# Performance work log

Hardware: AMD Instinct MI355X
Metric: run time of the kernel (lower is better)

The kernel has to match this reference:

```python
import jax, jax.numpy as jnp
import numpy as np

B, D, P, E, C = 2048, 4096, 64, 8, 64
K = D // P  # conv kernel = stride = input_dim / patch_num


def setup_inputs() -> dict:
    key = jax.random.key(0)
    k1, k2, k3, k4 = jax.random.split(key, 4)
    x = jax.random.normal(k1, (B, 1, D), jnp.float32)
    router_w = jax.random.normal(k2, (E, K), jnp.float32) * 0.02   # Router conv weight [E,1,K] squeezed
    expert_w = jax.random.normal(k3, (E, 2 * C, K), jnp.float32) * 0.001  # per-expert conv weights (small=True scaling)
    expert_b = jax.random.normal(k4, (E, 2 * C), jnp.float32) * 0.001
    return {"x": x, "router_w": router_w, "expert_w": expert_w, "expert_b": expert_b}


def reference(x, router_w, expert_w, expert_b):
    b, _, d = x.shape
    e, k = router_w.shape
    p = d // k
    c = expert_w.shape[1] // 2

    # Conv1d(1, ch, K, stride=K) == per-patch matmul; sum over dim 2 == sum over patches.
    patches = x.reshape(b, p, k)                                   # [B,P,K]

    # Router (eval mode: no noise)
    select = jnp.einsum('bpk,ek->be', patches, router_w)           # [B,E]

    # top1 routing
    gate = jnp.max(select, axis=-1)                                # [B]
    index = jnp.argmax(select, axis=-1)                            # [B]
    onehot = jax.nn.one_hot(index, e, dtype=select.dtype)          # [B,E]

    # aux load-balance loss
    density = onehot.mean(axis=0)
    density_proxy = select.mean(axis=0)
    loss = (density_proxy * density).mean() * float(e ** 2)

    # combine/dispatch (mask_flat is all ones for top1)
    combine = gate[:, None] * onehot                               # [B,E]
    dispatch = jax.lax.stop_gradient((combine != 0).astype(select.dtype))  # bool cast detaches grad
    select0 = dispatch

    # Dense dispatch: every expert sees the full batch, zero-masked by dispatch.
    # z[e,b,c,p] = conv of (dispatch[b,e]*x[b]) with expert e's kernel, + bias
    z = jnp.einsum('bpk,eck->ebcp', patches, expert_w)             # [E,B,2C,P]
    z = z * dispatch.T[:, :, None, None] + expert_b[:, None, :, None]
    z = z ** 3                                                     # nonlinear=True
    s = z.sum(axis=-1)                                             # sum over patches -> [E,B,2C]
    expert_out = jnp.stack([s[..., :c].sum(-1), s[..., c:].sum(-1)], axis=-1)  # [E,B,2]

    out = jnp.einsum('be,ebl->bl', combine, expert_out)            # [B,2]
    out = jax.nn.softmax(out, axis=1)
    return out, select0, loss
```

## Files before the change

### kernel.cpp

```cpp
#include <hip/hip_runtime.h>

#define BB 2048
#define DD 4096
#define PP 64
#define KK 64
#define EE 8
#define C2 128
#define NBLK (BB / 2)

typedef __attribute__((ext_vector_type(8))) short short8;
typedef __attribute__((ext_vector_type(4))) float floatx4;

__device__ inline unsigned pack2_trunc(float lo, float hi) {
    unsigned ul = __builtin_bit_cast(unsigned, lo);
    unsigned uh = __builtin_bit_cast(unsigned, hi);
    return (uh & 0xFFFF0000u) | (ul >> 16);
}

__global__ __launch_bounds__(256, 4) void moe_main(
    const float* __restrict__ x, const float* __restrict__ rw,
    const float* __restrict__ ew, const float* __restrict__ eb,
    float* __restrict__ out, float* __restrict__ ws)
{
    __shared__ float red[2][9];
    __shared__ float sh_h[4];
    const int lane = threadIdx.x & 63;
    const int w = threadIdx.x >> 6;
    const int half = w & 1;
    const int rowb = w >> 1;
    const int b = blockIdx.x * 2 + rowb;
    const int r = lane & 15, q = lane >> 4;
    const float* xb = x + (size_t)b * DD;

    float ps[16];
    #pragma unroll
    for (int j = 0; j < 16; ++j) ps[j] = 0.f;
    short8 af[8];
    #pragma unroll
    for (int mt = 0; mt < 4; ++mt) {
        #pragma unroll
        for (int kb = 0; kb < 2; ++kb) {
            const float* base = xb + (mt * 16 + r) * 64 + kb * 32 + q * 8;
            float4 v0 = *(const float4*)base;
            float4 v1 = *(const float4*)(base + 4);
            ps[kb*8+0] += v0.x; ps[kb*8+1] += v0.y; ps[kb*8+2] += v0.z; ps[kb*8+3] += v0.w;
            ps[kb*8+4] += v1.x; ps[kb*8+5] += v1.y; ps[kb*8+6] += v1.z; ps[kb*8+7] += v1.w;
            uint4 u;
            u.x = pack2_trunc(v0.x, v0.y); u.y = pack2_trunc(v0.z, v0.w);
            u.z = pack2_trunc(v1.x, v1.y); u.w = pack2_trunc(v1.z, v1.w);
            af[mt * 2 + kb] = __builtin_bit_cast(short8, u);
        }
    }

    float d[8];
    #pragma unroll
    for (int e2 = 0; e2 < 8; ++e2) {
        const float* rwe = rw + e2 * KK;
        float4 a0 = *(const float4*)(rwe + q * 8);
        float4 a1 = *(const float4*)(rwe + q * 8 + 4);
        float4 b0 = *(const float4*)(rwe + 32 + q * 8);
        float4 b1 = *(const float4*)(rwe + 32 + q * 8 + 4);
        float t = ps[0]*a0.x + ps[1]*a0.y + ps[2]*a0.z + ps[3]*a0.w
                + ps[4]*a1.x + ps[5]*a1.y + ps[6]*a1.z + ps[7]*a1.w
                + ps[8]*b0.x + ps[9]*b0.y + ps[10]*b0.z + ps[11]*b0.w
                + ps[12]*b1.x + ps[13]*b1.y + ps[14]*b1.z + ps[15]*b1.w;
        t += __shfl_xor(t, 1);  t += __shfl_xor(t, 2);  t += __shfl_xor(t, 4);
        t += __shfl_xor(t, 8);  t += __shfl_xor(t, 16); t += __shfl_xor(t, 32);
        d[e2] = t;
    }
    float gate = d[0]; int e = 0;
    #pragma unroll
    for (int e2 = 1; e2 < 8; ++e2)
        if (d[e2] > gate) { gate = d[e2]; e = e2; }

    if (lane == 0 && half == 0) {
        #pragma unroll
        for (int e2 = 0; e2 < 8; ++e2) red[rowb][e2] = d[e2];
        red[rowb][8] = (float)e;
        float on = (gate != 0.f) ? 1.f : 0.f;
        float4 o0 = make_float4(e==0?on:0.f, e==1?on:0.f, e==2?on:0.f, e==3?on:0.f);
        float4 o1 = make_float4(e==4?on:0.f, e==5?on:0.f, e==6?on:0.f, e==7?on:0.f);
        *(float4*)(out + BB * 2 + b * 8)     = o0;
        *(float4*)(out + BB * 2 + b * 8 + 4) = o1;
    }

    const float* we = ew + (size_t)e * (C2 * KK);
    float h = 0.f;
    #pragma unroll
    for (int ntl = 0; ntl < 4; ++ntl) {
        const int nt = half * 4 + ntl;
        float bs = eb[e * C2 + nt * 16 + r];
        const float* wr = we + (nt * 16 + r) * KK + q * 8;
        float4 w0 = *(const float4*)wr;
        float4 w1 = *(const float4*)(wr + 4);
        float4 w2 = *(const float4*)(wr + 32);
        float4 w3 = *(const float4*)(wr + 36);
        uint4 u0, u1;
        u0.x = pack2_trunc(w0.x, w0.y); u0.y = pack2_trunc(w0.z, w0.w);
        u0.z = pack2_trunc(w1.x, w1.y); u0.w = pack2_trunc(w1.z, w1.w);
        u1.x = pack2_trunc(w2.x, w2.y); u1.y = pack2_trunc(w2.z, w2.w);
        u1.z = pack2_trunc(w3.x, w3.y); u1.w = pack2_trunc(w3.z, w3.w);
        short8 bf0 = __builtin_bit_cast(short8, u0);
        short8 bf1 = __builtin_bit_cast(short8, u1);
        #pragma unroll
        for (int mt = 0; mt < 4; ++mt) {
            floatx4 a4 = (floatx4){0.f, 0.f, 0.f, 0.f};
            a4 = __builtin_amdgcn_mfma_f32_16x16x32_bf16(af[mt*2+0], bf0, a4, 0, 0, 0);
            a4 = __builtin_amdgcn_mfma_f32_16x16x32_bf16(af[mt*2+1], bf1, a4, 0, 0, 0);
            #pragma unroll
            for (int i = 0; i < 4; ++i) {
                float z = a4[i] + bs;
                h = fmaf(z * z, z, h);
            }
        }
    }
    #pragma unroll
    for (int off = 1; off < 64; off <<= 1)
        h += __shfl_xor(h, off);

    if (lane == 0) sh_h[w] = h;
    __syncthreads();

    if (half == 0 && lane == 0) {
        float l0 = gate * sh_h[w], l1 = gate * sh_h[w + 1];
        float m = fmaxf(l0, l1);
        float e0 = __expf(l0 - m), e1 = __expf(l1 - m);
        float inv = 1.f / (e0 + e1);
        float2 o; o.x = e0 * inv; o.y = e1 * inv;
        *(float2*)(out + b * 2) = o;
    }

    if (threadIdx.x < 8) {
        const int t = threadIdx.x;
        float sp = red[0][t] + red[1][t];
        float sc = ((red[0][8] == (float)t) ? 1.f : 0.f) + ((red[1][8] == (float)t) ? 1.f : 0.f);
        ws[blockIdx.x * 16 + t]     = sp;
        ws[blockIdx.x * 16 + 8 + t] = sc;
    }
}

__global__ __launch_bounds__(256) void loss2(
    const float* __restrict__ ws, float* __restrict__ out)
{
    __shared__ float red[4][16];
    const int t = threadIdx.x;
    const int w = t >> 6, lane = t & 63;

    float p[8] = {0,0,0,0,0,0,0,0};
    float c[8] = {0,0,0,0,0,0,0,0};
    #pragma unroll
    for (int it = 0; it < NBLK / 256; ++it) {
        const float4* row = (const float4*)(ws + (size_t)(it * 256 + t) * 16);
        float4 r0 = row[0], r1 = row[1], r2 = row[2], r3 = row[3];
        p[0] += r0.x; p[1] += r0.y; p[2] += r0.z; p[3] += r0.w;
        p[4] += r1.x; p[5] += r1.y; p[6] += r1.z; p[7] += r1.w;
        c[0] += r2.x; c[1] += r2.y; c[2] += r2.z; c[3] += r2.w;
        c[4] += r3.x; c[5] += r3.y; c[6] += r3.z; c[7] += r3.w;
    }
    #pragma unroll
    for (int off = 32; off > 0; off >>= 1) {
        #pragma unroll
        for (int e2 = 0; e2 < 8; ++e2) {
            p[e2] += __shfl_xor(p[e2], off);
            c[e2] += __shfl_xor(c[e2], off);
        }
    }
    if (lane == 0) {
        #pragma unroll
        for (int e2 = 0; e2 < 8; ++e2) { red[w][e2] = p[e2]; red[w][8 + e2] = c[e2]; }
    }
    __syncthreads();
    if (t == 0) {
        float loss = 0.f;
        #pragma unroll
        for (int e2 = 0; e2 < 8; ++e2) {
            float sp = red[0][e2] + red[1][e2] + red[2][e2] + red[3][e2];
            float sc = red[0][8 + e2] + red[1][8 + e2] + red[2][8 + e2] + red[3][8 + e2];
            loss += (sp * (1.f / BB)) * (sc * (1.f / BB));
        }
        out[BB * 2 + BB * 8] = loss * (float)EE;
    }
}

extern "C" void kernel_launch(void* const* d_in, const int* in_sizes, int n_in,
                              void* d_out, int out_size, void* d_ws, size_t ws_size,
                              hipStream_t stream) {
    (void)in_sizes; (void)n_in; (void)out_size; (void)ws_size;
    const float* x  = (const float*)d_in[0];
    const float* rw = (const float*)d_in[1];
    const float* ew = (const float*)d_in[2];
    const float* eb = (const float*)d_in[3];
    float* out = (float*)d_out;
    float* ws  = (float*)d_ws;

    moe_main<<<NBLK, 256, 0, stream>>>(x, rw, ew, eb, out, ws);
    loss2<<<1, 256, 0, stream>>>(ws, out);
}
```

Baseline: 96.17 us.

## Assign one batch row per block, splitting expert channels across four waves

Each block now handles a single batch row. All four waves split the 128 expert output channels, two 16-wide tiles each, where before two waves shared one row with four tiles each. The launch grid doubles to 2048 blocks, the occupancy hint rises to 8, and the per-block shared-memory reduction for loss partials is replaced by direct per-row workspace writes. The aim is more parallelism and less serial MFMA work per wave. In exchange, every wave now redoes the row load, bf16 packing and router dot products, so redundant x traffic and router work double, and loss2 reads twice as many workspace rows.

After: 134.1 us. 1.39x slower.

```diff
diff --git a/kernel.cpp b/kernel.cpp
--- a/kernel.cpp
+++ b/kernel.cpp
@@ -6,7 +6,7 @@
 #define KK 64
 #define EE 8
 #define C2 128
-#define NBLK (BB / 2)
+#define NBLK BB
 
 typedef __attribute__((ext_vector_type(8))) short short8;
 typedef __attribute__((ext_vector_type(4))) float floatx4;
@@ -17,18 +17,15 @@
     return (uh & 0xFFFF0000u) | (ul >> 16);
 }
 
-__global__ __launch_bounds__(256, 4) void moe_main(
+__global__ __launch_bounds__(256, 8) void moe_main(
     const float* __restrict__ x, const float* __restrict__ rw,
     const float* __restrict__ ew, const float* __restrict__ eb,
     float* __restrict__ out, float* __restrict__ ws)
 {
-    __shared__ float red[2][9];
     __shared__ float sh_h[4];
     const int lane = threadIdx.x & 63;
     const int w = threadIdx.x >> 6;
-    const int half = w & 1;
-    const int rowb = w >> 1;
-    const int b = blockIdx.x * 2 + rowb;
+    const int b = blockIdx.x;
     const int r = lane & 15, q = lane >> 4;
     const float* xb = x + (size_t)b * DD;
 
@@ -73,22 +70,18 @@
     for (int e2 = 1; e2 < 8; ++e2)
         if (d[e2] > gate) { gate = d[e2]; e = e2; }
 
-    if (lane == 0 && half == 0) {
-        #pragma unroll
-        for (int e2 = 0; e2 < 8; ++e2) red[rowb][e2] = d[e2];
-        red[rowb][8] = (float)e;
+    if (w == 0 && lane < 8) {
         float on = (gate != 0.f) ? 1.f : 0.f;
-        float4 o0 = make_float4(e==0?on:0.f, e==1?on:0.f, e==2?on:0.f, e==3?on:0.f);
-        float4 o1 = make_float4(e==4?on:0.f, e==5?on:0.f, e==6?on:0.f, e==7?on:0.f);
-        *(float4*)(out + BB * 2 + b * 8)     = o0;
-        *(float4*)(out + BB * 2 + b * 8 + 4) = o1;
+        out[BB * 2 + b * 8 + lane] = (lane == e) ? on : 0.f;
+        ws[b * 16 + lane]     = d[lane];
+        ws[b * 16 + 8 + lane] = (lane == e) ? 1.f : 0.f;
     }
 
     const float* we = ew + (size_t)e * (C2 * KK);
     float h = 0.f;
     #pragma unroll
-    for (int ntl = 0; ntl < 4; ++ntl) {
-        const int nt = half * 4 + ntl;
+    for (int ntl = 0; ntl < 2; ++ntl) {
+        const int nt = w * 2 + ntl;
         float bs = eb[e * C2 + nt * 16 + r];
         const float* wr = we + (nt * 16 + r) * KK + q * 8;
         float4 w0 = *(const float4*)wr;
@@ -121,21 +114,14 @@
     if (lane == 0) sh_h[w] = h;
     __syncthreads();
 
-    if (half == 0 && lane == 0) {
-        float l0 = gate * sh_h[w], l1 = gate * sh_h[w + 1];
+    if (threadIdx.x == 0) {
+        float l0 = gate * (sh_h[0] + sh_h[1]);
+        float l1 = gate * (sh_h[2] + sh_h[3]);
         float m = fmaxf(l0, l1);
         float e0 = __expf(l0 - m), e1 = __expf(l1 - m);
         float inv = 1.f / (e0 + e1);
         float2 o; o.x = e0 * inv; o.y = e1 * inv;
         *(float2*)(out + b * 2) = o;
-    }
-
-    if (threadIdx.x < 8) {
-        const int t = threadIdx.x;
-        float sp = red[0][t] + red[1][t];
-        float sc = ((red[0][8] == (float)t) ? 1.f : 0.f) + ((red[1][8] == (float)t) ? 1.f : 0.f);
-        ws[blockIdx.x * 16 + t]     = sp;
-        ws[blockIdx.x * 16 + 8 + t] = sc;
     }
 }
 
@@ -149,7 +135,7 @@
     float p[8] = {0,0,0,0,0,0,0,0};
     float c[8] = {0,0,0,0,0,0,0,0};
     #pragma unroll
-    for (int it = 0; it < NBLK / 256; ++it) {
+    for (int it = 0; it < BB / 256; ++it) {
         const float4* row = (const float4*)(ws + (size_t)(it * 256 + t) * 16);
         float4 r0 = row[0], r1 = row[1], r2 = row[2], r3 = row[3];
         p[0] += r0.x; p[1] += r0.y; p[2] += r0.z; p[3] += r0.w;
```
